# Kernel optimization log

Hardware: AMD Instinct MI355X
Metric: run time of the kernel (lower is better)

The kernel has to match this reference:

```python
import jax, jax.numpy as jnp
import numpy as np

N_NODE = 50000
EMB = 128
LAYERS = 2
B = 1024
L = 50
E = 1_600_000


def setup_inputs() -> dict:
    key = jax.random.key(0)
    ks = jax.random.split(key, 21)
    d = EMB
    stdv = 1.0 / np.sqrt(d)
    u = lambda k, shape: jax.random.uniform(k, shape, minval=-stdv, maxval=stdv, dtype=jnp.float32)
    inp = {
        'adj_row': jax.random.randint(ks[0], (E,), 0, N_NODE, dtype=jnp.int32),
        'adj_col': jax.random.randint(ks[1], (E,), 0, N_NODE, dtype=jnp.int32),
        'adj_val': jax.random.uniform(ks[2], (E,), dtype=jnp.float32) / 32.0,  # ~row-normalized sparse adjacency
        'embedding': jax.random.normal(ks[3], (N_NODE, d), dtype=jnp.float32) * 0.1,
        'session_item': jax.random.randint(ks[4], (B, L), 0, N_NODE, dtype=jnp.int32),  # 0 hits the zero pad row
        'session_len': jnp.full((B, 1), float(L), dtype=jnp.float32),
        'D': jax.random.uniform(ks[5], (B, B), dtype=jnp.float32) / B,
        'A_sess': jax.random.uniform(ks[6], (B, B), dtype=jnp.float32) / B,
        'A_gnn': jax.random.uniform(ks[7], (B, L, 2 * L), dtype=jnp.float32) / L,
        'alias_pos': jax.random.randint(ks[8], (B, L), 0, L, dtype=jnp.int32),
        'hidden': jax.random.normal(ks[9], (B, L, d), dtype=jnp.float32) * 0.1,
        'W_in': u(ks[10], (d, d)), 'b_in': u(ks[11], (d,)),
        'W_out': u(ks[12], (d, d)), 'b_out': u(ks[13], (d,)),
        'w_ih': u(ks[14], (3 * d, 2 * d)), 'b_ih': u(ks[15], (3 * d,)),
        'w_hh': u(ks[16], (3 * d, d)), 'b_hh': u(ks[17], (3 * d,)),
        'b_iah': u(ks[18], (d,)), 'b_oah': u(ks[19], (d,)),
    }
    return inp


def reference(adj_row, adj_col, adj_val, embedding, session_item, session_len,
              D, A_sess, A_gnn, alias_pos, hidden,
              W_in, b_in, W_out, b_out, w_ih, b_ih, w_hh, b_hh, b_iah, b_oah):
    # ---- HyperConv: layers of sparse (COO) adjacency @ embedding, summed over hops ----
    emb = embedding
    final = embedding
    for _ in range(LAYERS):
        emb = jax.ops.segment_sum(adj_val[:, None] * emb[adj_col], adj_row, num_segments=N_NODE)
        final = final + emb
    item_emb = final  # [N_NODE, d]

    # ---- LineConv: zero-padded gather + mean pool over session, then session-graph propagation ----
    pad_table = jnp.concatenate([jnp.zeros((1, EMB), embedding.dtype), embedding], axis=0)
    seq_h = pad_table[session_item]                      # [B, L, d]
    sess = jnp.sum(seq_h, axis=1) / session_len          # [B, d]
    DA = D @ A_sess                                      # [B, B]
    acc = sess
    s = sess
    for _ in range(LAYERS):
        s = DA @ s
        acc = acc + s
    session_emb = acc                                    # [B, d]

    # ---- GNN: gather per-session in/out adjacency rows, gated GRU-style update ----
    in_out = jnp.take_along_axis(A_gnn, alias_pos[:, :, None], axis=1)  # [B, L, 2L]
    h_in = hidden @ W_in.T + b_in
    h_out = hidden @ W_out.T + b_out
    input_in = jnp.einsum('bij,bjd->bid', in_out[:, :, :L], h_in) + b_iah
    input_out = jnp.einsum('bij,bjd->bid', in_out[:, :, L:], h_out) + b_oah
    inputs = jnp.concatenate([input_in, input_out], axis=2)             # [B, L, 2d]
    gi = inputs @ w_ih.T + b_ih
    gh = hidden @ w_hh.T + b_hh
    i_r, i_i, i_n = jnp.split(gi, 3, axis=2)
    h_r, h_i, h_n = jnp.split(gh, 3, axis=2)
    resetgate = jax.nn.sigmoid(i_r + h_r)
    inputgate = jax.nn.sigmoid(i_i + h_i)
    newgate = jnp.tanh(i_n + resetgate * h_n)
    hy = newgate + inputgate * (hidden - newgate)        # [B, L, d]

    return item_emb, session_emb, hy
```

## Files before the change

kernel.cpp:

```cpp
#include <hip/hip_runtime.h>

#define EMB 128
#define NN 50000
#define BB 1024
#define LL 50
#define NBK 49
#define NEB 512

typedef float f32x4 __attribute__((ext_vector_type(4)));
typedef float f32x2 __attribute__((ext_vector_type(2)));
typedef unsigned short u16;
typedef unsigned int u32;
typedef unsigned long long u64;
typedef u16 u16x4 __attribute__((ext_vector_type(4)));
typedef u32 u32x4 __attribute__((ext_vector_type(4)));
typedef short bf16x8 __attribute__((ext_vector_type(8)));

__device__ __forceinline__ float u2f(u16 u) {
    union { unsigned int i; float f; } v; v.i = ((unsigned int)u) << 16; return v.f;
}
__device__ __forceinline__ u16 f2b(float f) {
    union { float f; unsigned int i; } v; v.f = f;
    unsigned int i = v.i;
    return (u16)((i + 0x7FFFu + ((i >> 16) & 1u)) >> 16);
}
__device__ __forceinline__ float lo2f(u32 w) { return u2f((u16)(w & 0xffffu)); }
__device__ __forceinline__ float hi2f(u32 w) { return u2f((u16)(w >> 16)); }
__device__ __forceinline__ float sigmoidf_(float x) { return 1.f / (1.f + __expf(-x)); }

__device__ __forceinline__ bf16x8 ld_cvt8(const float* p) {
    f32x4 v0 = *(const f32x4*)p;
    f32x4 v1 = *(const f32x4*)(p + 4);
    union { u16 u[8]; bf16x8 b; } r;
#pragma unroll
    for (int t = 0; t < 4; t++) { r.u[t] = f2b(v0[t]); r.u[4 + t] = f2b(v1[t]); }
    return r.b;
}

__global__ __launch_bounds__(256) void prep_kernel(
    const float* __restrict__ emb, const float* __restrict__ A, const float* __restrict__ D,
    const float* __restrict__ wih, const float* __restrict__ whh,
    const float* __restrict__ Win, const float* __restrict__ Wout,
    u16* __restrict__ emb_bf, u16* __restrict__ A_bf, u16* __restrict__ D_bf,
    u16* __restrict__ wih_bf, u16* __restrict__ whh_bf,
    u16* __restrict__ Win_bf, u16* __restrict__ Wout_bf,
    const int* __restrict__ rowi, int* __restrict__ bcnt,
    int E, int chunk)
{
    __shared__ int lc[NBK];
    int gid = blockIdx.x * 256 + threadIdx.x;
    int stride = gridDim.x * 256;
    int tid = threadIdx.x;
    if (blockIdx.x < NEB) {
        if (tid < NBK) lc[tid] = 0;
        __syncthreads();
        int beg = blockIdx.x * chunk, end = min(E, beg + chunk);
        for (int e = beg + tid; e < end; e += 256)
            atomicAdd(&lc[rowi[e] >> 10], 1);
        __syncthreads();
        if (tid < NBK) bcnt[blockIdx.x * NBK + tid] = lc[tid];
    }
    for (int i = gid; i < 1600000; i += stride) {
        f32x4 v = *(const f32x4*)(emb + (size_t)i * 4);
        u16x4 p;
#pragma unroll
        for (int t = 0; t < 4; t++) p[t] = f2b(v[t]);
        *(u16x4*)(emb_bf + (size_t)i * 4) = p;
    }
    for (int i = gid; i < 2277376; i += stride) {
        const float* s; u16* d; int off;
        if (i < 1048576)      { s = A;    d = A_bf;    off = i; }
        else if (i < 2097152) { s = D;    d = D_bf;    off = i - 1048576; }
        else if (i < 2195456) { s = wih;  d = wih_bf;  off = i - 2097152; }
        else if (i < 2244608) { s = whh;  d = whh_bf;  off = i - 2195456; }
        else if (i < 2260992) { s = Win;  d = Win_bf;  off = i - 2244608; }
        else                  { s = Wout; d = Wout_bf; off = i - 2260992; }
        d[off] = f2b(s[off]);
    }
}

__global__ __launch_bounds__(512) void bktscan_kernel(
    const int* __restrict__ bcnt, int* __restrict__ sofs, int* __restrict__ btot)
{
    __shared__ int ps[512];
    int k = blockIdx.x, t = threadIdx.x;
    int c = bcnt[t * NBK + k];
    ps[t] = c; __syncthreads();
    for (int off = 1; off < 512; off <<= 1) {
        int v = (t >= off) ? ps[t - off] : 0;
        __syncthreads();
        ps[t] += v; __syncthreads();
    }
    sofs[t * NBK + k] = ps[t] - c;
    if (t == 511) btot[k] = ps[511];
}

__global__ __launch_bounds__(64) void btotal_kernel(
    const int* __restrict__ btot, int* __restrict__ bofs, int E)
{
    if (threadIdx.x == 0) {
        int run = 0;
        for (int k = 0; k < NBK; k++) { bofs[k] = run; run += btot[k]; }
        bofs[NBK] = E;
    }
}

__global__ __launch_bounds__(256) void emit_kernel(
    const int* __restrict__ rowi, const int* __restrict__ coli, const float* __restrict__ val,
    const int* __restrict__ sofs, const int* __restrict__ bofs,
    u64* __restrict__ egs, int E, int chunk)
{
    __shared__ int cur[NBK];
    int b = blockIdx.x, tid = threadIdx.x;
    if (tid < NBK) cur[tid] = bofs[tid] + sofs[b * NBK + tid];
    __syncthreads();
    int beg = b * chunk, end = min(E, beg + chunk);
    for (int e = beg + tid; e < end; e += 256) {
        int r = rowi[e];
        int slot = atomicAdd(&cur[r >> 10], 1);
        u64 entry = ((u64)(u32)(r & 1023) << 32)
                  | (u64)((u32)(u16)coli[e] | ((u32)f2b(val[e]) << 16));
        egs[slot] = entry;
    }
}

__global__ __launch_bounds__(1024) void binsort2_kernel(
    const u64* __restrict__ egs, const int* __restrict__ bofs,
    int* __restrict__ row_ptr, u32* __restrict__ eg, int E)
{
    __shared__ int cnt_s[1024];
    __shared__ int ps[1024];
    int k = blockIdx.x, tid = threadIdx.x;
    int r0 = k << 10;
    int beg = bofs[k], end = bofs[k + 1];
    cnt_s[tid] = 0;
    __syncthreads();
    for (int i = beg + tid; i < end; i += 1024)
        atomicAdd(&cnt_s[(int)(egs[i] >> 32)], 1);
    __syncthreads();
    int v = cnt_s[tid];
    ps[tid] = v; __syncthreads();
    for (int off = 1; off < 1024; off <<= 1) {
        int t = (tid >= off) ? ps[tid - off] : 0;
        __syncthreads();
        ps[tid] += t; __syncthreads();
    }
    int ex = beg + ps[tid] - v;
    if (r0 + tid <= NN) row_ptr[r0 + tid] = ex;
    if (k == NBK - 1 && tid == 1023) row_ptr[NN] = E;
    cnt_s[tid] = ex;
    __syncthreads();
    for (int i = beg + tid; i < end; i += 1024) {
        u64 entry = egs[i];
        int rlo = (int)(entry >> 32);
        int p = atomicAdd(&cnt_s[rlo], 1);
        eg[p] = (u32)entry;
    }
}

template<int FUSE>
__global__ __launch_bounds__(256) void gatherb_kernel(
    const int* __restrict__ row_ptr, const u32* __restrict__ eg,
    const u16* __restrict__ src, const float* __restrict__ emb0,
    u16* __restrict__ dst_bf, float* __restrict__ dst_f)
{
    int wave = threadIdx.x >> 6;
    int lane = threadIdx.x & 63;
    int g  = lane >> 4;
    int fl = lane & 15;
    int r = blockIdx.x * 4 + wave;
    if (r >= NN) return;
    int beg = row_ptr[r], end = row_ptr[r + 1];

    float acc[8];
#pragma unroll
    for (int t = 0; t < 8; t++) acc[t] = 0.f;

    if (beg < end) {
        int last = end - 1;
        int npair = (end - beg + 7) >> 3;
        u32 pkA = eg[min(beg + g, last)];
        u32 pkB = eg[min(beg + 4 + g, last)];
        float vA = (beg + g     < end) ? u2f((u16)(pkA >> 16)) : 0.f;
        float vB = (beg + 4 + g < end) ? u2f((u16)(pkB >> 16)) : 0.f;
        u32x4 xA = *(const u32x4*)(src + ((pkA & 0xffffu) << 7) + (fl << 3));
        u32x4 xB = *(const u32x4*)(src + ((pkB & 0xffffu) << 7) + (fl << 3));
        pkA = eg[min(beg + 8  + g, last)];
        pkB = eg[min(beg + 12 + g, last)];

        int e = beg;
        for (int p = 0; p < npair; p++) {
            float cvA = vA, cvB = vB;
            u32x4 cxA = xA, cxB = xB;
            int eN = e + 8;
            vA = (eN + g     < end) ? u2f((u16)(pkA >> 16)) : 0.f;
            vB = (eN + 4 + g < end) ? u2f((u16)(pkB >> 16)) : 0.f;
            xA = *(const u32x4*)(src + ((pkA & 0xffffu) << 7) + (fl << 3));
            xB = *(const u32x4*)(src + ((pkB & 0xffffu) << 7) + (fl << 3));
            int eS = e + 16;
            pkA = eg[min(eS + g, last)];
            pkB = eg[min(eS + 4 + g, last)];
#pragma unroll
            for (int t = 0; t < 4; t++) {
                acc[2 * t]     += cvA * lo2f(cxA[t]);
                acc[2 * t + 1] += cvA * hi2f(cxA[t]);
            }
#pragma unroll
            for (int t = 0; t < 4; t++) {
                acc[2 * t]     += cvB * lo2f(cxB[t]);
                acc[2 * t + 1] += cvB * hi2f(cxB[t]);
            }
            e += 8;
        }
    }

#pragma unroll
    for (int t = 0; t < 8; t++) {
        acc[t] += __shfl_xor(acc[t], 16);
        acc[t] += __shfl_xor(acc[t], 32);
    }

    if (lane < 16) {
        if (FUSE) {
            u32x4 s = *(const u32x4*)(src + ((u32)r << 7) + (lane << 3));
            const float* e0p = emb0 + ((size_t)r << 7) + (lane << 3);
            f32x4 e0a = *(const f32x4*)e0p;
            f32x4 e0b = *(const f32x4*)(e0p + 4);
            f32x4 o0, o1;
#pragma unroll
            for (int t = 0; t < 2; t++) {
                o0[2 * t]     = acc[2 * t]     + e0a[2 * t]     + lo2f(s[t]);
                o0[2 * t + 1] = acc[2 * t + 1] + e0a[2 * t + 1] + hi2f(s[t]);
                o1[2 * t]     = acc[4 + 2 * t]     + e0b[2 * t]     + lo2f(s[2 + t]);
                o1[2 * t + 1] = acc[4 + 2 * t + 1] + e0b[2 * t + 1] + hi2f(s[2 + t]);
            }
            float* dp = dst_f + ((size_t)r << 7) + (lane << 3);
            *(f32x4*)dp = o0;
            *(f32x4*)(dp + 4) = o1;
        } else {
            u32x4 w;
#pragma unroll
            for (int t = 0; t < 4; t++)
                w[t] = (u32)f2b(acc[2 * t]) | ((u32)f2b(acc[2 * t + 1]) << 16);
            *(u32x4*)(dst_bf + ((size_t)r << 7) + (lane << 3)) = w;
        }
    }
}

__global__ __launch_bounds__(128) void sess_pool_kernel(
    const int* __restrict__ items, const float* __restrict__ emb,
    const float* __restrict__ slen, float* __restrict__ sess, u16* __restrict__ sessT)
{
    int b = blockIdx.x, d = threadIdx.x;
    const int* it = items + b * LL;
    float acc = 0.f;
    for (int l = 0; l < LL; l++) {
        int idx = it[l];
        if (idx > 0) acc += emb[(size_t)(idx - 1) * EMB + d];
    }
    float v = acc / slen[b];
    sess[b * EMB + d] = v;
    sessT[d * BB + b] = f2b(v);
}

template<int WT, int WF>
__global__ __launch_bounds__(256) void mm_mfma_kernel(
    const u16* __restrict__ M_bf, const u16* __restrict__ Xt_bf,
    u16* __restrict__ Ct_bf, float* __restrict__ C_f)
{
    int tid = threadIdx.x;
    int wv = tid >> 6, lane = tid & 63, cl = lane & 15, kg = lane >> 4;
    int rbase = blockIdx.x * 16;
    f32x4 acc[2];
    acc[0] = (f32x4)0.f; acc[1] = (f32x4)0.f;
    const u16* arow = M_bf + (size_t)(rbase + cl) * BB + kg * 8;
    const u16* brow = Xt_bf + (size_t)(wv * 32 + cl) * BB + kg * 8;
#pragma unroll 4
    for (int k0 = 0; k0 < BB; k0 += 32) {
        bf16x8 a  = *(const bf16x8*)(arow + k0);
        bf16x8 b0 = *(const bf16x8*)(brow + k0);
        bf16x8 b1 = *(const bf16x8*)(brow + (size_t)16 * BB + k0);
        acc[0] = __builtin_amdgcn_mfma_f32_16x16x32_bf16(a, b0, acc[0], 0, 0, 0);
        acc[1] = __builtin_amdgcn_mfma_f32_16x16x32_bf16(a, b1, acc[1], 0, 0, 0);
    }
#pragma unroll
    for (int nt = 0; nt < 2; nt++) {
        int col = (wv * 2 + nt) * 16 + cl;
#pragma unroll
        for (int j = 0; j < 4; j++) {
            int row = rbase + kg * 4 + j;
            if (WF) C_f[(size_t)row * EMB + col] = acc[nt][j];
            if (WT) Ct_bf[(size_t)col * BB + row] = f2b(acc[nt][j]);
        }
    }
}

__global__ __launch_bounds__(256) void out1_kernel(
    const float* __restrict__ a, const float* __restrict__ b,
    const float* __restrict__ c, float* __restrict__ o, int n)
{
    int i = blockIdx.x * 256 + threadIdx.x;
    if (i < n) o[i] = a[i] + b[i] + c[i];
}

__global__ __launch_bounds__(256, 3) void gnn_tail_kernel(
    const float* __restrict__ hidden,
    const u16* __restrict__ W_in_bf, const u16* __restrict__ W_out_bf,
    const float* __restrict__ b_in, const float* __restrict__ b_out,
    const float* __restrict__ A_gnn, const int* __restrict__ alias_pos,
    const float* __restrict__ b_iah, const float* __restrict__ b_oah,
    const u16* __restrict__ w_ih_bf, const float* __restrict__ b_ih,
    const u16* __restrict__ w_hh_bf, const float* __restrict__ b_hh,
    float* __restrict__ hy)
{
    __shared__ __attribute__((aligned(16))) u16 AioHs[64 * 128];
    __shared__ __attribute__((aligned(16))) u16 hTsXs[256 * 72];
    int b = blockIdx.x;
    int tid = threadIdx.x;
    int wv = tid >> 6, lane = tid & 63, cl = lane & 15, kg = lane >> 4;

    for (int i = tid; i < 64 * 32; i += 256) {
        int row = i >> 5, c4 = i & 31;
        u16x4 p = (u16x4)0;
        if (row < LL) {
            int pos = alias_pos[b * LL + row];
            const float* ar = A_gnn + ((size_t)b * LL + pos) * (2 * LL);
#pragma unroll
            for (int t = 0; t < 4; t++) {
                int jp = c4 * 4 + t;
                int col = (jp < 64) ? jp : (50 + (jp - 64));
                int ok = (jp < 64) ? (jp < LL) : ((jp - 64) < LL);
                if (ok) p[t] = f2b(ar[col]);
            }
        }
        *(u16x4*)((char*)AioHs + row * 256 + ((c4 * 8) ^ ((row & 7) << 4))) = p;
    }

    {
        const float* hsrc = hidden + (size_t)b * LL * EMB;
        int mr = wv * 16 + cl;
        f32x4 acc1[16];
#pragma unroll
        for (int nt = 0; nt < 16; nt++) acc1[nt] = (f32x4)0.f;
#pragma unroll
        for (int ks = 0; ks < 4; ks++) {
            int k0 = ks * 32;
            bf16x8 a = (mr < LL) ? ld_cvt8(hsrc + mr * 128 + k0 + kg * 8) : (bf16x8)0;
#pragma unroll
            for (int nt = 0; nt < 16; nt++) {
                const u16* wsrc = (nt < 8) ? W_in_bf : W_out_bf;
                int wr = (nt & 7) * 16 + cl;
                bf16x8 bf = *(const bf16x8*)(wsrc + (size_t)wr * 128 + k0 + kg * 8);
                acc1[nt] = __builtin_amdgcn_mfma_f32_16x16x32_bf16(a, bf, acc1[nt], 0, 0, 0);
            }
        }
#pragma unroll
        for (int nt = 0; nt < 16; nt++) {
            int col = nt * 16 + cl;
            float bias = (col < 128) ? b_in[col] : b_out[col - 128];
            int r0 = wv * 16 + kg * 4;
            u16x4 p;
#pragma unroll
            for (int j = 0; j < 4; j++)
                p[j] = (r0 + j < LL) ? f2b(acc1[nt][j] + bias) : (u16)0;
            *(u16x4*)&hTsXs[col * 72 + r0] = p;
        }
    }
    __syncthreads();

    f32x4 acc[16];
#pragma unroll
    for (int nt = 0; nt < 16; nt++) acc[nt] = (f32x4)0.f;
#pragma unroll
    for (int ks = 0; ks < 2; ks++) {
#pragma unroll
        for (int nt = 0; nt < 16; nt++) {
            int koff = (nt < 8) ? 0 : 64;
            int k0 = koff + ks * 32;
            int mr = wv * 16 + cl;
            bf16x8 a = *(const bf16x8*)((const char*)AioHs + mr * 256 +
                        (((k0 << 1) + (kg << 4)) ^ ((mr & 7) << 4)));
            bf16x8 bf = *(const bf16x8*)&hTsXs[(nt * 16 + cl) * 72 + ks * 32 + kg * 8];
            acc[nt] = __builtin_amdgcn_mfma_f32_16x16x32_bf16(a, bf, acc[nt], 0, 0, 0);
        }
    }
    __syncthreads();

#pragma unroll
    for (int nt = 0; nt < 16; nt++) {
        int dp = nt * 16 + cl;
        float bias = (dp < 128) ? b_iah[dp] : b_oah[dp - 128];
#pragma unroll
        for (int j = 0; j < 4; j++) {
            int i = wv * 16 + kg * 4 + j;
            *(u16*)((char*)hTsXs + i * 512 + ((dp * 2) ^ ((i & 7) << 4))) =
                f2b(acc[nt][j] + bias);
        }
    }
    const float* hsrc = hidden + (size_t)b * LL * EMB;
#pragma unroll
    for (int i2 = 0; i2 < 8; i2++) {
        int lin = i2 * 256 + tid;
        int row = lin >> 5, c4 = lin & 31;
        u16x4 p = (u16x4)0;
        if (row < LL) {
            f32x4 v = *(const f32x4*)(hsrc + row * 128 + c4 * 4);
#pragma unroll
            for (int t = 0; t < 4; t++) p[t] = f2b(v[t]);
        }
        *(u16x4*)((char*)AioHs + row * 256 + ((c4 * 8) ^ ((row & 7) << 4))) = p;
    }
    __syncthreads();

    f32x4 acc_ri[4][2][2];
    f32x4 acc_n1[4][2];
    f32x4 acc_n2[4][2];
#pragma unroll
    for (int mt = 0; mt < 4; mt++)
#pragma unroll
        for (int t = 0; t < 2; t++) {
            acc_ri[mt][0][t] = (f32x4)0.f; acc_ri[mt][1][t] = (f32x4)0.f;
            acc_n1[mt][t] = (f32x4)0.f; acc_n2[mt][t] = (f32x4)0.f;
        }

#pragma unroll
    for (int ks = 0; ks < 8; ks++) {
        int k0 = ks * 32;
        bf16x8 a[4];
#pragma unroll
        for (int mt = 0; mt < 4; mt++) {
            int mr = mt * 16 + cl;
            a[mt] = *(const bf16x8*)((const char*)hTsXs + mr * 512 +
                     (((k0 << 1) + (kg << 4)) ^ ((mr & 7) << 4)));
        }
#pragma unroll
        for (int g = 0; g < 3; g++)
#pragma unroll
            for (int t = 0; t < 2; t++) {
                int brow = g * 128 + wv * 32 + t * 16 + cl;
                bf16x8 bw = *(const bf16x8*)(w_ih_bf + (size_t)brow * 256 + k0 + kg * 8);
#pragma unroll
                for (int mt = 0; mt < 4; mt++) {
                    f32x4* dst = (g < 2) ? &acc_ri[mt][g][t] : &acc_n1[mt][t];
                    *dst = __builtin_amdgcn_mfma_f32_16x16x32_bf16(a[mt], bw, *dst, 0, 0, 0);
                }
            }
    }
#pragma unroll
    for (int ks = 0; ks < 4; ks++) {
        int k0 = ks * 32;
        bf16x8 a[4];
#pragma unroll
        for (int mt = 0; mt < 4; mt++) {
            int mr = mt * 16 + cl;
            a[mt] = *(const bf16x8*)((const char*)AioHs + mr * 256 +
                     (((k0 << 1) + (kg << 4)) ^ ((mr & 7) << 4)));
        }
#pragma unroll
        for (int g = 0; g < 3; g++)
#pragma unroll
            for (int t = 0; t < 2; t++) {
                int brow = g * 128 + wv * 32 + t * 16 + cl;
                bf16x8 bw = *(const bf16x8*)(w_hh_bf + (size_t)brow * 128 + k0 + kg * 8);
#pragma unroll
                for (int mt = 0; mt < 4; mt++) {
                    f32x4* dst = (g < 2) ? &acc_ri[mt][g][t] : &acc_n2[mt][t];
                    *dst = __builtin_amdgcn_mfma_f32_16x16x32_bf16(a[mt], bw, *dst, 0, 0, 0);
                }
            }
    }

#pragma unroll
    for (int t = 0; t < 2; t++) {
        int d = wv * 32 + t * 16 + cl;
        float br = b_ih[d] + b_hh[d];
        float bi = b_ih[128 + d] + b_hh[128 + d];
        float bn1 = b_ih[256 + d], bn2 = b_hh[256 + d];
#pragma unroll
        for (int mt = 0; mt < 4; mt++)
#pragma unroll
            for (int j = 0; j < 4; j++) {
                int row = mt * 16 + kg * 4 + j;
                if (row >= LL) continue;
                float rg = sigmoidf_(acc_ri[mt][0][t][j] + br);
                float ig = sigmoidf_(acc_ri[mt][1][t][j] + bi);
                float ng = tanhf(acc_n1[mt][t][j] + bn1 + rg * (acc_n2[mt][t][j] + bn2));
                u16 hb = *(const u16*)((const char*)AioHs + row * 256 + ((d * 2) ^ ((row & 7) << 4)));
                float h = u2f(hb);
                hy[((size_t)b * LL + row) * 128 + d] = ng + ig * (h - ng);
            }
    }
}

extern "C" void kernel_launch(void* const* d_in, const int* in_sizes, int n_in,
                              void* d_out, int out_size, void* d_ws, size_t ws_size,
                              hipStream_t stream) {
    (void)n_in; (void)out_size; (void)ws_size;
    const int*   adj_row      = (const int*)d_in[0];
    const int*   adj_col      = (const int*)d_in[1];
    const float* adj_val      = (const float*)d_in[2];
    const float* embedding    = (const float*)d_in[3];
    const int*   session_item = (const int*)d_in[4];
    const float* session_len  = (const float*)d_in[5];
    const float* Dm           = (const float*)d_in[6];
    const float* A_sess       = (const float*)d_in[7];
    const float* A_gnn        = (const float*)d_in[8];
    const int*   alias_pos    = (const int*)d_in[9];
    const float* hidden       = (const float*)d_in[10];
    const float* W_in         = (const float*)d_in[11];
    const float* b_in         = (const float*)d_in[12];
    const float* W_out        = (const float*)d_in[13];
    const float* b_out        = (const float*)d_in[14];
    const float* w_ih         = (const float*)d_in[15];
    const float* b_ih         = (const float*)d_in[16];
    const float* w_hh         = (const float*)d_in[17];
    const float* b_hh         = (const float*)d_in[18];
    const float* b_iah        = (const float*)d_in[19];
    const float* b_oah        = (const float*)d_in[20];
    const int E = in_sizes[0];

    float* out0 = (float*)d_out;
    float* out1 = out0 + 6400000;
    float* out2 = out1 + 131072;

    float* ws = (float*)d_ws;
    u16*  emb_bf  = (u16*)ws;
    int*  bcnt  = (int*)(ws + 3200000);
    int*  sofs  = (int*)(ws + 3230000);
    int*  btot  = (int*)(ws + 3260000);
    u16*  accA_bf = (u16*)(ws + 3200000);
    u32*  eg    = (u32*)(ws + 6400000);
    u64*  egs   = (u64*)(ws + 8000000);
    float* sess  = ws + 11200000;
    u16*   sessT = (u16*)(ws + 11350000);
    u16*   t1T   = (u16*)(ws + 11400000);
    u16*   s1T   = (u16*)(ws + 11450000);
    u16*   t2T   = (u16*)(ws + 11500000);
    float* s1    = ws + 11550000;
    float* s2    = ws + 11700000;
    u16*   A_bf  = (u16*)(ws + 11850000);
    u16*   D_bf  = (u16*)(ws + 12400000);
    int*   row_ptr = (int*)(ws + 12950000);
    int*   bofs    = row_ptr + NN + 1;
    u16* w_ih_bf   = (u16*)(ws + 13107200);
    u16* w_hh_bf   = w_ih_bf + 98304;
    u16* W_in_bf   = w_hh_bf + 49152;
    u16* W_out_bf  = W_in_bf + 16384;

    int chunk = (E + NEB - 1) / NEB;

    prep_kernel<<<2048, 256, 0, stream>>>(embedding, A_sess, Dm, w_ih, w_hh, W_in, W_out,
                                          emb_bf, A_bf, D_bf, w_ih_bf, w_hh_bf, W_in_bf, W_out_bf,
                                          adj_row, bcnt, E, chunk);

    bktscan_kernel<<<NBK, 512, 0, stream>>>(bcnt, sofs, btot);
    btotal_kernel<<<1, 64, 0, stream>>>(btot, bofs, E);
    emit_kernel<<<NEB, 256, 0, stream>>>(adj_row, adj_col, adj_val, sofs, bofs, egs, E, chunk);
    binsort2_kernel<<<NBK, 1024, 0, stream>>>(egs, bofs, row_ptr, eg, E);
    gatherb_kernel<0><<<(NN + 3) / 4, 256, 0, stream>>>(row_ptr, eg, emb_bf, embedding, accA_bf, (float*)nullptr);
    gatherb_kernel<1><<<(NN + 3) / 4, 256, 0, stream>>>(row_ptr, eg, accA_bf, embedding, (u16*)nullptr, out0);

    sess_pool_kernel<<<BB, 128, 0, stream>>>(session_item, embedding, session_len, sess, sessT);
    mm_mfma_kernel<1, 0><<<64, 256, 0, stream>>>(A_bf, sessT, t1T, (float*)nullptr);
    mm_mfma_kernel<1, 1><<<64, 256, 0, stream>>>(D_bf, t1T, s1T, s1);
    mm_mfma_kernel<1, 0><<<64, 256, 0, stream>>>(A_bf, s1T, t2T, (float*)nullptr);
    mm_mfma_kernel<0, 1><<<64, 256, 0, stream>>>(D_bf, t2T, (u16*)nullptr, s2);
    out1_kernel<<<(131072 + 255) / 256, 256, 0, stream>>>(sess, s1, s2, out1, 131072);

    gnn_tail_kernel<<<BB, 256, 0, stream>>>(hidden, W_in_bf, W_out_bf, b_in, b_out,
                                            A_gnn, alias_pos, b_iah, b_oah,
                                            w_ih_bf, b_ih, w_hh_bf, b_hh, out2);
}
```

Baseline: 376.6 us.

## Split GNN tail kernel across 8 waves and prefetch A_gnn rows

The GRU tail kernel now runs 512 threads per block instead of 256. Each wave handles half the output columns of the first two GEMMs and 16 instead of 32 output features in the gate GEMMs, which cuts per-thread accumulator registers. The alias-gathered A_gnn rows are loaded into registers before the first GEMM and written to shared memory afterwards, so their global latency overlaps the W_in/W_out matmul. The trade-off is more waves per block sharing the same LDS, and the min-blocks hint from the launch bounds is dropped.

```diff
diff --git a/kernel.cpp b/kernel.cpp
--- a/kernel.cpp
+++ b/kernel.cpp
@@ -303,7 +303,7 @@
     if (i < n) o[i] = a[i] + b[i] + c[i];
 }
 
-__global__ __launch_bounds__(256, 3) void gnn_tail_kernel(
+__global__ __launch_bounds__(512) void gnn_tail_kernel(
     const float* __restrict__ hidden,
     const u16* __restrict__ W_in_bf, const u16* __restrict__ W_out_bf,
     const float* __restrict__ b_in, const float* __restrict__ b_out,
@@ -318,47 +318,52 @@
     int b = blockIdx.x;
     int tid = threadIdx.x;
     int wv = tid >> 6, lane = tid & 63, cl = lane & 15, kg = lane >> 4;
-
-    for (int i = tid; i < 64 * 32; i += 256) {
-        int row = i >> 5, c4 = i & 31;
-        u16x4 p = (u16x4)0;
-        if (row < LL) {
-            int pos = alias_pos[b * LL + row];
-            const float* ar = A_gnn + ((size_t)b * LL + pos) * (2 * LL);
-#pragma unroll
-            for (int t = 0; t < 4; t++) {
-                int jp = c4 * 4 + t;
-                int col = (jp < 64) ? jp : (50 + (jp - 64));
-                int ok = (jp < 64) ? (jp < LL) : ((jp - 64) < LL);
-                if (ok) p[t] = f2b(ar[col]);
-            }
-        }
-        *(u16x4*)((char*)AioHs + row * 256 + ((c4 * 8) ^ ((row & 7) << 4))) = p;
+    int wr = wv & 3;
+    int wh = wv >> 2;
+
+    int pr_row[4], pr_c4[4], ppos[4];
+#pragma unroll
+    for (int it = 0; it < 4; it++) {
+        int i = tid + it * 512;
+        pr_row[it] = i >> 5; pr_c4[it] = i & 31;
+        ppos[it] = (pr_row[it] < LL) ? alias_pos[b * LL + pr_row[it]] : 0;
+    }
+    float av[4][4];
+#pragma unroll
+    for (int it = 0; it < 4; it++) {
+        const float* ar = A_gnn + ((size_t)b * LL + ppos[it]) * (2 * LL);
+#pragma unroll
+        for (int t = 0; t < 4; t++) {
+            int jp = pr_c4[it] * 4 + t;
+            int col = (jp < 64) ? jp : (50 + (jp - 64));
+            int ok = (pr_row[it] < LL) && ((jp < 64) ? (jp < LL) : ((jp - 64) < LL));
+            av[it][t] = ok ? ar[col] : 0.f;
+        }
     }
 
     {
         const float* hsrc = hidden + (size_t)b * LL * EMB;
-        int mr = wv * 16 + cl;
-        f32x4 acc1[16];
-#pragma unroll
-        for (int nt = 0; nt < 16; nt++) acc1[nt] = (f32x4)0.f;
+        int mr = wr * 16 + cl;
+        const u16* wsrc = wh ? W_out_bf : W_in_bf;
+        f32x4 acc1[8];
+#pragma unroll
+        for (int nt = 0; nt < 8; nt++) acc1[nt] = (f32x4)0.f;
 #pragma unroll
         for (int ks = 0; ks < 4; ks++) {
             int k0 = ks * 32;
             bf16x8 a = (mr < LL) ? ld_cvt8(hsrc + mr * 128 + k0 + kg * 8) : (bf16x8)0;
 #pragma unroll
-            for (int nt = 0; nt < 16; nt++) {
-                const u16* wsrc = (nt < 8) ? W_in_bf : W_out_bf;
-                int wr = (nt & 7) * 16 + cl;
-                bf16x8 bf = *(const bf16x8*)(wsrc + (size_t)wr * 128 + k0 + kg * 8);
+            for (int nt = 0; nt < 8; nt++) {
+                int wrow = nt * 16 + cl;
+                bf16x8 bf = *(const bf16x8*)(wsrc + (size_t)wrow * 128 + k0 + kg * 8);
                 acc1[nt] = __builtin_amdgcn_mfma_f32_16x16x32_bf16(a, bf, acc1[nt], 0, 0, 0);
             }
         }
 #pragma unroll
-        for (int nt = 0; nt < 16; nt++) {
-            int col = nt * 16 + cl;
+        for (int nt = 0; nt < 8; nt++) {
+            int col = (wh * 8 + nt) * 16 + cl;
             float bias = (col < 128) ? b_in[col] : b_out[col - 128];
-            int r0 = wv * 16 + kg * 4;
+            int r0 = wr * 16 + kg * 4;
             u16x4 p;
 #pragma unroll
             for (int j = 0; j < 4; j++)
@@ -366,62 +371,70 @@
             *(u16x4*)&hTsXs[col * 72 + r0] = p;
         }
     }
-    __syncthreads();
-
-    f32x4 acc[16];
-#pragma unroll
-    for (int nt = 0; nt < 16; nt++) acc[nt] = (f32x4)0.f;
+
+#pragma unroll
+    for (int it = 0; it < 4; it++) {
+        u16x4 p;
+#pragma unroll
+        for (int t = 0; t < 4; t++) p[t] = f2b(av[it][t]);
+        *(u16x4*)((char*)AioHs + pr_row[it] * 256 + ((pr_c4[it] * 8) ^ ((pr_row[it] & 7) << 4))) = p;
+    }
+    __syncthreads();
+
+    f32x4 acc[8];
+#pragma unroll
+    for (int nt = 0; nt < 8; nt++) acc[nt] = (f32x4)0.f;
 #pragma unroll
     for (int ks = 0; ks < 2; ks++) {
 #pragma unroll
-        for (int nt = 0; nt < 16; nt++) {
-            int koff = (nt < 8) ? 0 : 64;
-            int k0 = koff + ks * 32;
-            int mr = wv * 16 + cl;
+        for (int nt8 = 0; nt8 < 8; nt8++) {
+            int nt = wh * 8 + nt8;
+            int k0 = wh * 64 + ks * 32;
+            int mr = wr * 16 + cl;
             bf16x8 a = *(const bf16x8*)((const char*)AioHs + mr * 256 +
                         (((k0 << 1) + (kg << 4)) ^ ((mr & 7) << 4)));
             bf16x8 bf = *(const bf16x8*)&hTsXs[(nt * 16 + cl) * 72 + ks * 32 + kg * 8];
-            acc[nt] = __builtin_amdgcn_mfma_f32_16x16x32_bf16(a, bf, acc[nt], 0, 0, 0);
-        }
-    }
-    __syncthreads();
-
-#pragma unroll
-    for (int nt = 0; nt < 16; nt++) {
-        int dp = nt * 16 + cl;
+            acc[nt8] = __builtin_amdgcn_mfma_f32_16x16x32_bf16(a, bf, acc[nt8], 0, 0, 0);
+        }
+    }
+    __syncthreads();
+
+#pragma unroll
+    for (int nt8 = 0; nt8 < 8; nt8++) {
+        int dp = (wh * 8 + nt8) * 16 + cl;
         float bias = (dp < 128) ? b_iah[dp] : b_oah[dp - 128];
 #pragma unroll
         for (int j = 0; j < 4; j++) {
-            int i = wv * 16 + kg * 4 + j;
+            int i = wr * 16 + kg * 4 + j;
             *(u16*)((char*)hTsXs + i * 512 + ((dp * 2) ^ ((i & 7) << 4))) =
-                f2b(acc[nt][j] + bias);
-        }
-    }
-    const float* hsrc = hidden + (size_t)b * LL * EMB;
-#pragma unroll
-    for (int i2 = 0; i2 < 8; i2++) {
-        int lin = i2 * 256 + tid;
-        int row = lin >> 5, c4 = lin & 31;
-        u16x4 p = (u16x4)0;
-        if (row < LL) {
-            f32x4 v = *(const f32x4*)(hsrc + row * 128 + c4 * 4);
-#pragma unroll
-            for (int t = 0; t < 4; t++) p[t] = f2b(v[t]);
-        }
-        *(u16x4*)((char*)AioHs + row * 256 + ((c4 * 8) ^ ((row & 7) << 4))) = p;
-    }
-    __syncthreads();
-
-    f32x4 acc_ri[4][2][2];
-    f32x4 acc_n1[4][2];
-    f32x4 acc_n2[4][2];
-#pragma unroll
-    for (int mt = 0; mt < 4; mt++)
-#pragma unroll
-        for (int t = 0; t < 2; t++) {
-            acc_ri[mt][0][t] = (f32x4)0.f; acc_ri[mt][1][t] = (f32x4)0.f;
-            acc_n1[mt][t] = (f32x4)0.f; acc_n2[mt][t] = (f32x4)0.f;
-        }
+                f2b(acc[nt8][j] + bias);
+        }
+    }
+    {
+        const float* hsrc = hidden + (size_t)b * LL * EMB;
+#pragma unroll
+        for (int i2 = 0; i2 < 4; i2++) {
+            int lin = i2 * 512 + tid;
+            int row = lin >> 5, c4 = lin & 31;
+            u16x4 p = (u16x4)0;
+            if (row < LL) {
+                f32x4 v = *(const f32x4*)(hsrc + row * 128 + c4 * 4);
+#pragma unroll
+                for (int t = 0; t < 4; t++) p[t] = f2b(v[t]);
+            }
+            *(u16x4*)((char*)AioHs + row * 256 + ((c4 * 8) ^ ((row & 7) << 4))) = p;
+        }
+    }
+    __syncthreads();
+
+    f32x4 acc_ri[4][2];
+    f32x4 acc_n1[4];
+    f32x4 acc_n2[4];
+#pragma unroll
+    for (int mt = 0; mt < 4; mt++) {
+        acc_ri[mt][0] = (f32x4)0.f; acc_ri[mt][1] = (f32x4)0.f;
+        acc_n1[mt] = (f32x4)0.f; acc_n2[mt] = (f32x4)0.f;
+    }
 
 #pragma unroll
     for (int ks = 0; ks < 8; ks++) {
@@ -434,17 +447,15 @@
                      (((k0 << 1) + (kg << 4)) ^ ((mr & 7) << 4)));
         }
 #pragma unroll
-        for (int g = 0; g < 3; g++)
-#pragma unroll
-            for (int t = 0; t < 2; t++) {
-                int brow = g * 128 + wv * 32 + t * 16 + cl;
-                bf16x8 bw = *(const bf16x8*)(w_ih_bf + (size_t)brow * 256 + k0 + kg * 8);
-#pragma unroll
-                for (int mt = 0; mt < 4; mt++) {
-                    f32x4* dst = (g < 2) ? &acc_ri[mt][g][t] : &acc_n1[mt][t];
-                    *dst = __builtin_amdgcn_mfma_f32_16x16x32_bf16(a[mt], bw, *dst, 0, 0, 0);
-                }
-            }
+        for (int g = 0; g < 3; g++) {
+            int brow = g * 128 + wv * 16 + cl;
+            bf16x8 bw = *(const bf16x8*)(w_ih_bf + (size_t)brow * 256 + k0 + kg * 8);
+#pragma unroll
+            for (int mt = 0; mt < 4; mt++) {
+                f32x4* dst = (g < 2) ? &acc_ri[mt][g] : &acc_n1[mt];
+                *dst = __builtin_amdgcn_mfma_f32_16x16x32_bf16(a[mt], bw, *dst, 0, 0, 0);
+            }
+        }
     }
 #pragma unroll
     for (int ks = 0; ks < 4; ks++) {
@@ -457,22 +468,19 @@
                      (((k0 << 1) + (kg << 4)) ^ ((mr & 7) << 4)));
         }
 #pragma unroll
-        for (int g = 0; g < 3; g++)
-#pragma unroll
-            for (int t = 0; t < 2; t++) {
-                int brow = g * 128 + wv * 32 + t * 16 + cl;
-                bf16x8 bw = *(const bf16x8*)(w_hh_bf + (size_t)brow * 128 + k0 + kg * 8);
-#pragma unroll
-                for (int mt = 0; mt < 4; mt++) {
-                    f32x4* dst = (g < 2) ? &acc_ri[mt][g][t] : &acc_n2[mt][t];
-                    *dst = __builtin_amdgcn_mfma_f32_16x16x32_bf16(a[mt], bw, *dst, 0, 0, 0);
-                }
-            }
-    }
-
-#pragma unroll
-    for (int t = 0; t < 2; t++) {
-        int d = wv * 32 + t * 16 + cl;
+        for (int g = 0; g < 3; g++) {
+            int brow = g * 128 + wv * 16 + cl;
+            bf16x8 bw = *(const bf16x8*)(w_hh_bf + (size_t)brow * 128 + k0 + kg * 8);
+#pragma unroll
+            for (int mt = 0; mt < 4; mt++) {
+                f32x4* dst = (g < 2) ? &acc_ri[mt][g] : &acc_n2[mt];
+                *dst = __builtin_amdgcn_mfma_f32_16x16x32_bf16(a[mt], bw, *dst, 0, 0, 0);
+            }
+        }
+    }
+
+    {
+        int d = wv * 16 + cl;
         float br = b_ih[d] + b_hh[d];
         float bi = b_ih[128 + d] + b_hh[128 + d];
         float bn1 = b_ih[256 + d], bn2 = b_hh[256 + d];
@@ -482,9 +490,9 @@
             for (int j = 0; j < 4; j++) {
                 int row = mt * 16 + kg * 4 + j;
                 if (row >= LL) continue;
-                float rg = sigmoidf_(acc_ri[mt][0][t][j] + br);
-                float ig = sigmoidf_(acc_ri[mt][1][t][j] + bi);
-                float ng = tanhf(acc_n1[mt][t][j] + bn1 + rg * (acc_n2[mt][t][j] + bn2));
+                float rg = sigmoidf_(acc_ri[mt][0][j] + br);
+                float ig = sigmoidf_(acc_ri[mt][1][j] + bi);
+                float ng = tanhf(acc_n1[mt][j] + bn1 + rg * (acc_n2[mt][j] + bn2));
                 u16 hb = *(const u16*)((const char*)AioHs + row * 256 + ((d * 2) ^ ((row & 7) << 4)));
                 float h = u2f(hb);
                 hy[((size_t)b * LL + row) * 128 + d] = ng + ig * (h - ng);
@@ -567,7 +575,7 @@
     mm_mfma_kernel<0, 1><<<64, 256, 0, stream>>>(D_bf, t2T, (u16*)nullptr, s2);
     out1_kernel<<<(131072 + 255) / 256, 256, 0, stream>>>(sess, s1, s2, out1, 131072);
 
-    gnn_tail_kernel<<<BB, 256, 0, stream>>>(hidden, W_in_bf, W_out_bf, b_in, b_out,
+    gnn_tail_kernel<<<BB, 512, 0, stream>>>(hidden, W_in_bf, W_out_bf, b_in, b_out,
                                             A_gnn, alias_pos, b_iah, b_oah,
                                             w_ih_bf, b_ih, w_hh_bf, b_hh, out2);
 }
```

After: 327.5 us. 13.0% less time.
